# Performance work log

Measured on AMD Instinct MI355X. Metric: run time of the kernel, lower is better.

## Reference

```python
import jax, jax.numpy as jnp
import numpy as np

B, C, L, D = 8, 32, 2048, 128
R, H = 8, 4  # num_routers, num_heads


def setup_inputs() -> dict:
    key = jax.random.key(0)
    ks = jax.random.split(key, 20)
    p = lambda k, shape: jax.random.normal(k, shape, dtype=jnp.float32) * 0.02
    inp = {
        "Z": jax.random.normal(ks[0], (B, C, L, D), dtype=jnp.float32),
        "router": p(ks[1], (R, D)),
        # router_sender projections (d_model -> d_model, torch Linear stored as x@W+b)
        "Wq1": p(ks[2], (D, D)), "bq1": jnp.zeros((D,), jnp.float32),
        "Wk1": p(ks[3], (D, D)), "bk1": jnp.zeros((D,), jnp.float32),
        "Wv1": p(ks[4], (D, D)), "bv1": jnp.zeros((D,), jnp.float32),
        "Wo1": p(ks[5], (D, D)), "bo1": jnp.zeros((D,), jnp.float32),
        # router_receiver projections
        "Wq2": p(ks[6], (D, D)), "bq2": jnp.zeros((D,), jnp.float32),
        "Wk2": p(ks[7], (D, D)), "bk2": jnp.zeros((D,), jnp.float32),
        "Wv2": p(ks[8], (D, D)), "bv2": jnp.zeros((D,), jnp.float32),
        "Wo2": p(ks[9], (D, D)), "bo2": jnp.zeros((D,), jnp.float32),
        # LayerNorm
        "gamma": jnp.ones((D,), jnp.float32),
        "beta": jnp.zeros((D,), jnp.float32),
    }
    return inp


def _cross_attn(q_in, k_in, v_in, Wq, bq, Wk, bk, Wv, bv, Wo, bo):
    # Informer FullAttention + AttentionLayer (dropout=0)
    Bn, Lq, Dm = q_in.shape
    Lk = k_in.shape[1]
    dh = Dm // H
    q = (q_in @ Wq + bq).reshape(Bn, Lq, H, dh)
    k = (k_in @ Wk + bk).reshape(Bn, Lk, H, dh)
    v = (v_in @ Wv + bv).reshape(Bn, Lk, H, dh)
    scale = 1.0 / np.sqrt(dh)
    scores = jnp.einsum("blhe,bshe->bhls", q, k) * scale
    A = jax.nn.softmax(scores, axis=-1)
    out = jnp.einsum("bhls,bshd->blhd", A, v).reshape(Bn, Lq, Dm)
    return out @ Wo + bo


def _layernorm(x, gamma, beta, eps=1e-5):
    mu = jnp.mean(x, axis=-1, keepdims=True)
    var = jnp.mean(jnp.square(x - mu), axis=-1, keepdims=True)
    return (x - mu) * jax.lax.rsqrt(var + eps) * gamma + beta


def reference(Z, router, Wq1, bq1, Wk1, bk1, Wv1, bv1, Wo1, bo1,
              Wq2, bq2, Wk2, bk2, Wv2, bv2, Wo2, bo2, gamma, beta):
    Bz, Cz, Lz, Dz = Z.shape
    x = Z.reshape(Bz * Cz, Lz, Dz)
    batch_router = jnp.broadcast_to(router[None], (Bz * Cz, R, Dz))
    # stage 1: routers attend to the sequence (R x L)
    router_buffer = _cross_attn(batch_router, x, x,
                                Wq1, bq1, Wk1, bk1, Wv1, bv1, Wo1, bo1)
    # stage 2: sequence attends to routers (L x R)
    router_receive = _cross_attn(x, router_buffer, router_buffer,
                                 Wq2, bq2, Wk2, bk2, Wv2, bv2, Wo2, bo2)
    out = _layernorm(x + router_receive, gamma, beta)
    return out.reshape(Bz, Cz, Lz, Dz)
```

## Files before the change

kernel.cpp:

```cpp
#include <hip/hip_runtime.h>

typedef float f4_t __attribute__((ext_vector_type(4)));
typedef __bf16 bf8_t __attribute__((ext_vector_type(8)));
typedef __bf16 bf4_t __attribute__((ext_vector_type(4)));

#define MFMA16(a,b,c) __builtin_amdgcn_mfma_f32_16x16x32_bf16((a),(b),(c),0,0,0)

static constexpr float kScale = 0.17677669529663687f;

__device__ __forceinline__ void bar_lds() {
  asm volatile("s_waitcnt lgkmcnt(0)" ::: "memory");
  __builtin_amdgcn_s_barrier();
}

__global__ __launch_bounds__(256) void k0_fold(
    const float* __restrict__ router, const float* __restrict__ Wq1,
    const float* __restrict__ bq1, const float* __restrict__ Wk1,
    const float* __restrict__ bk1, __bf16* __restrict__ q1t,
    float* __restrict__ c1)
{
  __shared__ float q1[8][128];
  const int t = threadIdx.x, b = blockIdx.x;
  for (int idx = t; idx < 1024; idx += 256) {
    int r = idx >> 7, dp = idx & 127;
    float acc = bq1[dp];
    for (int e = 0; e < 128; ++e) acc += router[r*128 + e] * Wq1[e*128 + dp];
    q1[r][dp] = acc;
  }
  __syncthreads();
  {
    int j = t & 31, h = j >> 3, r = j & 7;
    int e = b*8 + (t >> 5);
    float qv[32];
#pragma unroll
    for (int d = 0; d < 32; ++d) qv[d] = q1[r][h*32 + d];
    float acc = 0.f;
#pragma unroll
    for (int d = 0; d < 32; ++d) acc += qv[d] * Wk1[e*128 + h*32 + d];
    q1t[j*128 + e] = (__bf16)(acc * kScale);
  }
  if (b == 0 && t < 32) {
    int h = t >> 3, r = t & 7;
    float acc = 0.f;
    for (int d = 0; d < 32; ++d) acc += q1[r][h*32 + d] * bk1[h*32 + d];
    c1[t] = acc * kScale;
  }
}

__global__ __launch_bounds__(512) void k1_stage1(
    const float* __restrict__ Z, const __bf16* __restrict__ q1t_g,
    const float* __restrict__ c1_g, float* __restrict__ xap,
    float* __restrict__ lp, __bf16* __restrict__ xws)
{
  __shared__ __bf16 xb[64][136];
  __shared__ __bf16 xT[128][72];
  __shared__ __bf16 PT[32][72];
  __shared__ float lds_l[32];

  const int tid = threadIdx.x;
  const int bid = blockIdx.x;
  const float* xbase = Z + (size_t)bid * (256 * 128);
  __bf16* xwb = xws + (size_t)bid * (256 * 128);

  if (tid < 32) lds_l[tid] = 0.f;

  const int lane = tid & 63;
  const int w = tid >> 6;
  const int lc = lane & 15;
  const int lg = lane >> 4;
  const int ms = w >> 2;
  const int ns = w & 3;
  float c1v[4];
#pragma unroll
  for (int r2 = 0; r2 < 4; ++r2) c1v[r2] = c1_g[ms*16 + lg*4 + r2];
  bf8_t aq[4];
#pragma unroll
  for (int ks = 0; ks < 4; ++ks)
    aq[ks] = *(const bf8_t*)(q1t_g + (ms*16 + lc)*128 + ks*32 + lg*8);

  const f4_t fzero = {0.f, 0.f, 0.f, 0.f};
  f4_t accxa[2] = { fzero, fzero };
  float Lacc[4] = {0.f, 0.f, 0.f, 0.f};

  const int srow = tid >> 4;
  const int sd0  = (tid & 15) << 3;

  f4_t zr[4];
#pragma unroll
  for (int i = 0; i < 2; ++i) {
    const float* p = xbase + (srow + 32*i)*128 + sd0;
    zr[i*2]   = __builtin_nontemporal_load((const f4_t*)p);
    zr[i*2+1] = __builtin_nontemporal_load((const f4_t*)(p + 4));
  }

  bar_lds();

  for (int tile = 0; tile < 4; ++tile) {
#pragma unroll
    for (int i = 0; i < 2; ++i) {
      int pos = srow + 32*i;
      f4_t v0 = zr[i*2], v1 = zr[i*2+1];
      bf8_t b8 = { (__bf16)v0.x, (__bf16)v0.y, (__bf16)v0.z, (__bf16)v0.w,
                   (__bf16)v1.x, (__bf16)v1.y, (__bf16)v1.z, (__bf16)v1.w };
      *(bf8_t*)&xb[pos][sd0] = b8;
      *(bf8_t*)(xwb + (tile*64 + pos)*128 + sd0) = b8;
    }
    bar_lds();

    if (tile < 3) {
      const float* xt = xbase + (tile + 1) * (64 * 128);
#pragma unroll
      for (int i = 0; i < 2; ++i) {
        const float* p = xt + (srow + 32*i)*128 + sd0;
        zr[i*2]   = __builtin_nontemporal_load((const f4_t*)p);
        zr[i*2+1] = __builtin_nontemporal_load((const f4_t*)(p + 4));
      }
    }

#pragma unroll
    for (int s = 0; s < 2; ++s) {
      int u = tid + s*512;
      int dim = u & 127, pb = (u >> 7) << 3;
      bf8_t t8;
#pragma unroll
      for (int p = 0; p < 8; ++p) t8[p] = xb[pb + p][dim];
      *(bf8_t*)&xT[dim][pb] = t8;
    }
    f4_t sacc = fzero;
#pragma unroll
    for (int ks = 0; ks < 4; ++ks) {
      bf8_t b = *(const bf8_t*)&xb[ns*16 + lc][ks*32 + lg*8];
      sacc = MFMA16(aq[ks], b, sacc);
    }
    const int posn = ns*16 + lc;
#pragma unroll
    for (int r2 = 0; r2 < 4; ++r2) {
      float p = __expf(sacc[r2] + c1v[r2]);
      Lacc[r2] += p;
      PT[ms*16 + lg*4 + r2][posn] = (__bf16)p;
    }
    bar_lds();

#pragma unroll
    for (int nt = 0; nt < 2; ++nt) {
      const int dimt = (ns << 1) + nt;
#pragma unroll
      for (int ks = 0; ks < 2; ++ks) {
        bf8_t a = *(const bf8_t*)&xT[dimt*16 + lc][ks*32 + lg*8];
        bf8_t b = *(const bf8_t*)&PT[ms*16 + lc][ks*32 + lg*8];
        accxa[nt] = MFMA16(a, b, accxa[nt]);
      }
    }
  }

#pragma unroll
  for (int r2 = 0; r2 < 4; ++r2) {
    float v = Lacc[r2];
    v += __shfl_xor(v, 1);
    v += __shfl_xor(v, 2);
    v += __shfl_xor(v, 4);
    v += __shfl_xor(v, 8);
    if (lc == 0) atomicAdd(&lds_l[ms*16 + lg*4 + r2], v);
  }
  bar_lds();

  float* xo = xap + (size_t)bid * 4096;
  const int jrow = ms*16 + lc;
#pragma unroll
  for (int nt = 0; nt < 2; ++nt) {
    const int dim0 = ((ns << 1) + nt)*16 + lg*4;
    *(f4_t*)(xo + jrow*128 + dim0) = accxa[nt];
  }
  if (tid < 32) lp[bid*32 + tid] = lds_l[tid];
}

__global__ __launch_bounds__(256) void k1b_mid(
    const float* __restrict__ xap, const float* __restrict__ lp,
    const float* __restrict__ Wv1, const float* __restrict__ bv1,
    const float* __restrict__ Wo1, const float* __restrict__ bo1,
    const float* __restrict__ Wk2, const float* __restrict__ bk2,
    const float* __restrict__ Wv2, const float* __restrict__ bv2,
    const float* __restrict__ Wq2, const float* __restrict__ bq2,
    const float* __restrict__ Wo2,
    __bf16* __restrict__ kt2, float* __restrict__ c2, __bf16* __restrict__ vt2)
{
  __shared__ float xa[32][129];
  __shared__ float invl[32];
  __shared__ float out1[8][128];
  __shared__ float rb[8][128];
  __shared__ float k2s[8][128];
  __shared__ float v2s[8][128];

  const int t = threadIdx.x, b = blockIdx.x;
  for (int idx = t; idx < 4096; idx += 256) {
    float s = 0.f;
#pragma unroll
    for (int k = 0; k < 8; ++k)
      s += xap[(size_t)(b*8 + k) * 4096 + idx];
    xa[idx >> 7][idx & 127] = s;
  }
  if (t < 32) {
    float s = 0.f;
#pragma unroll
    for (int k = 0; k < 8; ++k) s += lp[(b*8 + k)*32 + t];
    invl[t] = 1.f / s;
  }
  bar_lds();

  for (int idx = t; idx < 1024; idx += 256) {
    int r = idx >> 7, hd = idx & 127, h = hd >> 5;
    int j = h*8 + r;
    float acc = 0.f;
    for (int e = 0; e < 128; ++e) acc += xa[j][e] * Wv1[e*128 + hd];
    out1[r][hd] = acc * invl[j] + bv1[hd];
  }
  bar_lds();
  for (int idx = t; idx < 1024; idx += 256) {
    int r = idx >> 7, e2 = idx & 127;
    float acc = bo1[e2];
    for (int hd = 0; hd < 128; ++hd) acc += out1[r][hd] * Wo1[hd*128 + e2];
    rb[r][e2] = acc;
  }
  bar_lds();
  for (int idx = t; idx < 2048; idx += 256) {
    int sel = idx >> 10;
    int r = (idx >> 7) & 7, hd = idx & 127;
    const float* W = sel ? Wv2 : Wk2;
    const float* bb = sel ? bv2 : bk2;
    float acc = bb[hd];
    for (int e = 0; e < 128; ++e) acc += rb[r][e] * W[e*128 + hd];
    float (*dst)[128] = sel ? v2s : k2s;
    dst[r][hd] = acc;
  }
  bar_lds();
  {
    const int j = t & 31, h = j >> 3, r = j & 7;
    const int esub = t >> 5;
    float k2v[32], v2v[32];
#pragma unroll
    for (int d = 0; d < 32; ++d) {
      k2v[d] = k2s[r][h*32 + d];
      v2v[d] = v2s[r][h*32 + d];
    }
#pragma unroll
    for (int ei = 0; ei < 16; ++ei) {
      const int e = esub + ei*8;
      float acck = 0.f, accv = 0.f;
#pragma unroll
      for (int d = 0; d < 32; ++d) {
        acck += Wq2[e*128 + h*32 + d] * k2v[d];
        accv += v2v[d] * Wo2[(h*32 + d)*128 + e];
      }
      kt2[(size_t)b*4096 + j*128 + e] = (__bf16)(acck * kScale);
      vt2[(size_t)b*4096 + e*32 + j] = (__bf16)accv;
    }
  }
  if (t < 32) {
    int h = t >> 3, r = t & 7;
    float acc = 0.f;
    for (int d = 0; d < 32; ++d) acc += bq2[h*32 + d] * k2s[r][h*32 + d];
    c2[b*32 + t] = acc * kScale;
  }
}

__global__ __launch_bounds__(512) void k2_stage2(
    const __bf16* __restrict__ xws, const __bf16* __restrict__ kt2,
    const float* __restrict__ c2g, const __bf16* __restrict__ vt2,
    const float* __restrict__ bo2, const float* __restrict__ gamma,
    const float* __restrict__ beta, float* __restrict__ out)
{
  __shared__ __bf16 xb[128][136];
  __shared__ __bf16 P2[128][40];

  const int tid = threadIdx.x;
  const int blk = blockIdx.x;
  const int batch = blk >> 1;

  const __bf16* ktb = kt2 + (size_t)batch * 4096;
  const __bf16* vtb = vt2 + (size_t)batch * 4096;

  const int lane = tid & 63;
  const int w = tid >> 6;
  const int lc = lane & 15;
  const int lg = lane >> 4;

  float c2v[2] = { c2g[batch*32 + lc], c2g[batch*32 + 16 + lc] };
  f4_t bo2v[8], gv[8], bv[8];
#pragma unroll
  for (int nt = 0; nt < 8; ++nt) {
    int dd = nt*16 + lg*4;
    bo2v[nt] = *(const f4_t*)(bo2 + dd);
    gv[nt]   = *(const f4_t*)(gamma + dd);
    bv[nt]   = *(const f4_t*)(beta + dd);
  }
  bf8_t vfrag[8];
#pragma unroll
  for (int nt = 0; nt < 8; ++nt)
    vfrag[nt] = *(const bf8_t*)(vtb + (nt*16 + lc)*32 + lg*8);

  int spos[4], sd[4];
#pragma unroll
  for (int j = 0; j < 4; ++j) {
    int c = lane + j*64;
    spos[j] = w*16 + (c >> 4);
    sd[j]   = (c & 15) << 3;
  }

  const size_t base0 = (size_t)blk * 8 * 16384;
  uint4 zx[4];
#pragma unroll
  for (int j = 0; j < 4; ++j)
    zx[j] = *(const uint4*)(xws + base0 + spos[j]*128 + sd[j]);

  const f4_t fzero = {0.f, 0.f, 0.f, 0.f};

  for (int c = 0; c < 8; ++c) {
    const size_t cb = base0 + (size_t)c * 16384;
#pragma unroll
    for (int j = 0; j < 4; ++j)
      *(uint4*)&xb[spos[j]][sd[j]] = zx[j];
    if (c < 7) {
#pragma unroll
      for (int j = 0; j < 4; ++j)
        zx[j] = *(const uint4*)(xws + cb + 16384 + spos[j]*128 + sd[j]);
    }

    f4_t sacc[2] = { fzero, fzero };
#pragma unroll
    for (int ks = 0; ks < 4; ++ks) {
      bf8_t a = *(const bf8_t*)&xb[w*16 + lc][ks*32 + lg*8];
#pragma unroll
      for (int nt = 0; nt < 2; ++nt) {
        bf8_t b = *(const bf8_t*)(ktb + (nt*16 + lc)*128 + ks*32 + lg*8);
        sacc[nt] = MFMA16(a, b, sacc[nt]);
      }
    }
#pragma unroll
    for (int nt = 0; nt < 2; ++nt) {
#pragma unroll
      for (int r2 = 0; r2 < 4; ++r2) {
        float p = __expf(sacc[nt][r2] + c2v[nt]);
        float sum = p;
        sum += __shfl_xor(sum, 1);
        sum += __shfl_xor(sum, 2);
        sum += __shfl_xor(sum, 4);
        P2[w*16 + lg*4 + r2][nt*16 + lc] = (__bf16)(p * __builtin_amdgcn_rcpf(sum));
      }
    }

    bf8_t pf = *(const bf8_t*)&P2[w*16 + lc][lg*8];
    f4_t racc[8];
#pragma unroll
    for (int nt = 0; nt < 8; ++nt)
      racc[nt] = MFMA16(vfrag[nt], pf, fzero);

    const int pos = w*16 + lc;
    float s1 = 0.f, s2 = 0.f;
#pragma unroll
    for (int nt = 0; nt < 8; ++nt) {
      bf4_t xq = *(const bf4_t*)&xb[pos][nt*16 + lg*4];
#pragma unroll
      for (int r = 0; r < 4; ++r) {
        float tv = racc[nt][r] + bo2v[nt][r] + (float)xq[r];
        racc[nt][r] = tv;
        s1 += tv; s2 += tv*tv;
      }
    }
    s1 += __shfl_xor(s1, 16); s1 += __shfl_xor(s1, 32);
    s2 += __shfl_xor(s2, 16); s2 += __shfl_xor(s2, 32);
    float mean = s1 * (1.f/128.f);
    float var = s2 * (1.f/128.f) - mean*mean;
    float rstd = rsqrtf(var + 1e-5f);

    float* y = out + cb + (size_t)pos*128;
#pragma unroll
    for (int nt = 0; nt < 8; ++nt) {
      f4_t o;
#pragma unroll
      for (int r = 0; r < 4; ++r)
        o[r] = (racc[nt][r] - mean) * rstd * gv[nt][r] + bv[nt][r];
      __builtin_nontemporal_store(o, (f4_t*)(y + nt*16 + lg*4));
    }
  }
}

extern "C" void kernel_launch(void* const* d_in, const int* in_sizes, int n_in,
                              void* d_out, int out_size, void* d_ws, size_t ws_size,
                              hipStream_t stream)
{
  const float* Z     = (const float*)d_in[0];
  const float* router= (const float*)d_in[1];
  const float* Wq1   = (const float*)d_in[2];
  const float* bq1   = (const float*)d_in[3];
  const float* Wk1   = (const float*)d_in[4];
  const float* bk1   = (const float*)d_in[5];
  const float* Wv1   = (const float*)d_in[6];
  const float* bv1   = (const float*)d_in[7];
  const float* Wo1   = (const float*)d_in[8];
  const float* bo1   = (const float*)d_in[9];
  const float* Wq2   = (const float*)d_in[10];
  const float* bq2   = (const float*)d_in[11];
  const float* Wk2   = (const float*)d_in[12];
  const float* bk2   = (const float*)d_in[13];
  const float* Wv2   = (const float*)d_in[14];
  const float* bv2   = (const float*)d_in[15];
  const float* Wo2   = (const float*)d_in[16];
  const float* bo2   = (const float*)d_in[17];
  const float* gamma = (const float*)d_in[18];
  const float* beta  = (const float*)d_in[19];
  float* out = (float*)d_out;

  char* base = (char*)d_ws;
  __bf16* q1tb = (__bf16*)(base);
  float*  c1   = (float*)(base + 8192);
  float*  c2   = (float*)(base + 16384);
  float*  lp   = (float*)(base + 65536);
  float*  xap  = (float*)(base + (1u<<20));
  __bf16* kt2b = (__bf16*)(base + (36u<<20));
  __bf16* vt2b = (__bf16*)(base + (38u<<20));
  __bf16* xws  = (__bf16*)(base + (40u<<20));
  (void)in_sizes; (void)n_in; (void)out_size; (void)ws_size;

  k0_fold<<<dim3(16), dim3(256), 0, stream>>>(router, Wq1, bq1, Wk1, bk1, q1tb, c1);
  k1_stage1<<<dim3(2048), dim3(512), 0, stream>>>(Z, q1tb, c1, xap, lp, xws);
  k1b_mid<<<dim3(256), dim3(256), 0, stream>>>(xap, lp, Wv1, bv1, Wo1, bo1,
                                               Wk2, bk2, Wv2, bv2, Wq2, bq2, Wo2,
                                               kt2b, c2, vt2b);
  k2_stage2<<<dim3(512), dim3(512), 0, stream>>>(xws, kt2b, c2, vt2b, bo2, gamma, beta, out);
}
```

Before: 283.6 us.

## Fuse mid-stage router projections into stage-2 kernel, keep K/V in LDS

Merges the per-batch router projection kernel into the stage-2 attention kernel. Each stage-2 block recomputes that batch's router buffer, K2 and V2 projections into shared memory and reads them from LDS instead of global workspace. This removes one kernel launch and the global round-trip of kt2/vt2/c2. In exchange, the two blocks of each batch both recompute the small projection work, and shared-memory use rises to about 64KB, which may lower occupancy.

```diff
diff --git a/kernel.cpp b/kernel.cpp
--- a/kernel.cpp
+++ b/kernel.cpp
@@ -174,40 +174,70 @@
   if (tid < 32) lp[bid*32 + tid] = lds_l[tid];
 }
 
-__global__ __launch_bounds__(256) void k1b_mid(
-    const float* __restrict__ xap, const float* __restrict__ lp,
+__global__ __launch_bounds__(512) void k2_stage2(
+    const __bf16* __restrict__ xws, const float* __restrict__ xap,
+    const float* __restrict__ lp,
     const float* __restrict__ Wv1, const float* __restrict__ bv1,
     const float* __restrict__ Wo1, const float* __restrict__ bo1,
     const float* __restrict__ Wk2, const float* __restrict__ bk2,
     const float* __restrict__ Wv2, const float* __restrict__ bv2,
     const float* __restrict__ Wq2, const float* __restrict__ bq2,
-    const float* __restrict__ Wo2,
-    __bf16* __restrict__ kt2, float* __restrict__ c2, __bf16* __restrict__ vt2)
+    const float* __restrict__ Wo2, const float* __restrict__ bo2,
+    const float* __restrict__ gamma, const float* __restrict__ beta,
+    float* __restrict__ out)
 {
-  __shared__ float xa[32][129];
-  __shared__ float invl[32];
-  __shared__ float out1[8][128];
-  __shared__ float rb[8][128];
-  __shared__ float k2s[8][128];
-  __shared__ float v2s[8][128];
-
-  const int t = threadIdx.x, b = blockIdx.x;
-  for (int idx = t; idx < 4096; idx += 256) {
+  __shared__ __align__(16) char smem[64256];
+  __bf16 (*xb)[136]  = (__bf16 (*)[136])(smem);
+  __bf16 (*P2)[40]   = (__bf16 (*)[40])(smem + 34816);
+  __bf16 (*ktL)[136] = (__bf16 (*)[136])(smem + 45056);
+  __bf16 (*vtL)[40]  = (__bf16 (*)[40])(smem + 53760);
+  float* c2L  = (float*)(smem + 64000);
+  float* invl = (float*)(smem + 64128);
+  float (*xa)[129]  = (float (*)[129])(smem);
+  float (*out1)[128] = (float (*)[128])(smem + 16512);
+  float (*rb)[128]   = (float (*)[128])(smem + 20608);
+  float (*k2s)[128]  = (float (*)[128])(smem + 24704);
+  float (*v2s)[128]  = (float (*)[128])(smem + 28800);
+
+  const int tid = threadIdx.x;
+  const int blk = blockIdx.x;
+  const int batch = blk >> 1;
+
+  const int lane = tid & 63;
+  const int w = tid >> 6;
+  const int lc = lane & 15;
+  const int lg = lane >> 4;
+
+  int spos[4], sd[4];
+#pragma unroll
+  for (int j = 0; j < 4; ++j) {
+    int c = lane + j*64;
+    spos[j] = w*16 + (c >> 4);
+    sd[j]   = (c & 15) << 3;
+  }
+  const size_t base0 = (size_t)blk * 8 * 16384;
+  uint4 zx[4];
+#pragma unroll
+  for (int j = 0; j < 4; ++j)
+    zx[j] = *(const uint4*)(xws + base0 + spos[j]*128 + sd[j]);
+
+#pragma unroll
+  for (int i = 0; i < 8; ++i) {
+    int idx = tid + i*512;
     float s = 0.f;
 #pragma unroll
     for (int k = 0; k < 8; ++k)
-      s += xap[(size_t)(b*8 + k) * 4096 + idx];
+      s += xap[(size_t)(batch*8 + k) * 4096 + idx];
     xa[idx >> 7][idx & 127] = s;
   }
-  if (t < 32) {
+  if (tid < 32) {
     float s = 0.f;
 #pragma unroll
-    for (int k = 0; k < 8; ++k) s += lp[(b*8 + k)*32 + t];
-    invl[t] = 1.f / s;
-  }
-  bar_lds();
-
-  for (int idx = t; idx < 1024; idx += 256) {
+    for (int k = 0; k < 8; ++k) s += lp[(batch*8 + k)*32 + tid];
+    invl[tid] = 1.f / s;
+  }
+  bar_lds();
+  for (int idx = tid; idx < 1024; idx += 512) {
     int r = idx >> 7, hd = idx & 127, h = hd >> 5;
     int j = h*8 + r;
     float acc = 0.f;
@@ -215,14 +245,14 @@
     out1[r][hd] = acc * invl[j] + bv1[hd];
   }
   bar_lds();
-  for (int idx = t; idx < 1024; idx += 256) {
+  for (int idx = tid; idx < 1024; idx += 512) {
     int r = idx >> 7, e2 = idx & 127;
     float acc = bo1[e2];
     for (int hd = 0; hd < 128; ++hd) acc += out1[r][hd] * Wo1[hd*128 + e2];
     rb[r][e2] = acc;
   }
   bar_lds();
-  for (int idx = t; idx < 2048; idx += 256) {
+  for (int idx = tid; idx < 2048; idx += 512) {
     int sel = idx >> 10;
     int r = (idx >> 7) & 7, hd = idx & 127;
     const float* W = sel ? Wv2 : Wk2;
@@ -234,8 +264,8 @@
   }
   bar_lds();
   {
-    const int j = t & 31, h = j >> 3, r = j & 7;
-    const int esub = t >> 5;
+    const int j = tid & 31, h = j >> 3, r = j & 7;
+    const int esub = tid >> 5;
     float k2v[32], v2v[32];
 #pragma unroll
     for (int d = 0; d < 32; ++d) {
@@ -243,48 +273,28 @@
       v2v[d] = v2s[r][h*32 + d];
     }
 #pragma unroll
-    for (int ei = 0; ei < 16; ++ei) {
-      const int e = esub + ei*8;
+    for (int ei = 0; ei < 8; ++ei) {
+      const int e = esub + ei*16;
       float acck = 0.f, accv = 0.f;
 #pragma unroll
       for (int d = 0; d < 32; ++d) {
         acck += Wq2[e*128 + h*32 + d] * k2v[d];
         accv += v2v[d] * Wo2[(h*32 + d)*128 + e];
       }
-      kt2[(size_t)b*4096 + j*128 + e] = (__bf16)(acck * kScale);
-      vt2[(size_t)b*4096 + e*32 + j] = (__bf16)accv;
-    }
-  }
-  if (t < 32) {
-    int h = t >> 3, r = t & 7;
-    float acc = 0.f;
-    for (int d = 0; d < 32; ++d) acc += bq2[h*32 + d] * k2s[r][h*32 + d];
-    c2[b*32 + t] = acc * kScale;
-  }
-}
-
-__global__ __launch_bounds__(512) void k2_stage2(
-    const __bf16* __restrict__ xws, const __bf16* __restrict__ kt2,
-    const float* __restrict__ c2g, const __bf16* __restrict__ vt2,
-    const float* __restrict__ bo2, const float* __restrict__ gamma,
-    const float* __restrict__ beta, float* __restrict__ out)
-{
-  __shared__ __bf16 xb[128][136];
-  __shared__ __bf16 P2[128][40];
-
-  const int tid = threadIdx.x;
-  const int blk = blockIdx.x;
-  const int batch = blk >> 1;
-
-  const __bf16* ktb = kt2 + (size_t)batch * 4096;
-  const __bf16* vtb = vt2 + (size_t)batch * 4096;
-
-  const int lane = tid & 63;
-  const int w = tid >> 6;
-  const int lc = lane & 15;
-  const int lg = lane >> 4;
-
-  float c2v[2] = { c2g[batch*32 + lc], c2g[batch*32 + 16 + lc] };
+      ktL[j][e] = (__bf16)(acck * kScale);
+      vtL[e][j] = (__bf16)accv;
+    }
+    if (tid < 32) {
+      int hh = tid >> 3, rr = tid & 7;
+      float acc = 0.f;
+#pragma unroll
+      for (int d = 0; d < 32; ++d) acc += bq2[hh*32 + d] * k2s[rr][hh*32 + d];
+      c2L[tid] = acc * kScale;
+    }
+  }
+  bar_lds();
+
+  float c2v[2] = { c2L[lc], c2L[16 + lc] };
   f4_t bo2v[8], gv[8], bv[8];
 #pragma unroll
   for (int nt = 0; nt < 8; ++nt) {
@@ -296,21 +306,7 @@
   bf8_t vfrag[8];
 #pragma unroll
   for (int nt = 0; nt < 8; ++nt)
-    vfrag[nt] = *(const bf8_t*)(vtb + (nt*16 + lc)*32 + lg*8);
-
-  int spos[4], sd[4];
-#pragma unroll
-  for (int j = 0; j < 4; ++j) {
-    int c = lane + j*64;
-    spos[j] = w*16 + (c >> 4);
-    sd[j]   = (c & 15) << 3;
-  }
-
-  const size_t base0 = (size_t)blk * 8 * 16384;
-  uint4 zx[4];
-#pragma unroll
-  for (int j = 0; j < 4; ++j)
-    zx[j] = *(const uint4*)(xws + base0 + spos[j]*128 + sd[j]);
+    vfrag[nt] = *(const bf8_t*)&vtL[nt*16 + lc][lg*8];
 
   const f4_t fzero = {0.f, 0.f, 0.f, 0.f};
 
@@ -331,7 +327,7 @@
       bf8_t a = *(const bf8_t*)&xb[w*16 + lc][ks*32 + lg*8];
 #pragma unroll
       for (int nt = 0; nt < 2; ++nt) {
-        bf8_t b = *(const bf8_t*)(ktb + (nt*16 + lc)*128 + ks*32 + lg*8);
+        bf8_t b = *(const bf8_t*)&ktL[nt*16 + lc][ks*32 + lg*8];
         sacc[nt] = MFMA16(a, b, sacc[nt]);
       }
     }
@@ -413,18 +409,16 @@
   char* base = (char*)d_ws;
   __bf16* q1tb = (__bf16*)(base);
   float*  c1   = (float*)(base + 8192);
-  float*  c2   = (float*)(base + 16384);
   float*  lp   = (float*)(base + 65536);
   float*  xap  = (float*)(base + (1u<<20));
-  __bf16* kt2b = (__bf16*)(base + (36u<<20));
-  __bf16* vt2b = (__bf16*)(base + (38u<<20));
   __bf16* xws  = (__bf16*)(base + (40u<<20));
   (void)in_sizes; (void)n_in; (void)out_size; (void)ws_size;
 
   k0_fold<<<dim3(16), dim3(256), 0, stream>>>(router, Wq1, bq1, Wk1, bk1, q1tb, c1);
   k1_stage1<<<dim3(2048), dim3(512), 0, stream>>>(Z, q1tb, c1, xap, lp, xws);
-  k1b_mid<<<dim3(256), dim3(256), 0, stream>>>(xap, lp, Wv1, bv1, Wo1, bo1,
-                                               Wk2, bk2, Wv2, bv2, Wq2, bq2, Wo2,
-                                               kt2b, c2, vt2b);
-  k2_stage2<<<dim3(512), dim3(512), 0, stream>>>(xws, kt2b, c2, vt2b, bo2, gamma, beta, out);
+  k2_stage2<<<dim3(512), dim3(512), 0, stream>>>(xws, xap, lp,
+                                                 Wv1, bv1, Wo1, bo1,
+                                                 Wk2, bk2, Wv2, bv2,
+                                                 Wq2, bq2, Wo2,
+                                                 bo2, gamma, beta, out);
 }
```

Result: slower. 305.1 us (+7.6%).
